# Optimization experiments

Measured on AMD Instinct MI355X. Metric: run time of the kernel, lower is better.

Reference implementation:

```python
import jax, jax.numpy as jnp
import numpy as np

EMBED = 1024
HEADS = 16
HEAD_DIM = EMBED // HEADS


def setup_inputs() -> dict:
    key = jax.random.key(0)
    ks = jax.random.split(key, 8)
    N, S = 4, 2048
    return {
        "keys": jax.random.normal(ks[0], (N, S, EMBED), dtype=jnp.float32),
        "query": jax.random.normal(ks[1], (N, S, EMBED), dtype=jnp.float32),
        "values": jax.random.normal(ks[2], (N, S, EMBED), dtype=jnp.float32),
        "Wk": jax.random.normal(ks[3], (HEAD_DIM, HEAD_DIM), dtype=jnp.float32) / np.sqrt(HEAD_DIM),
        "Wq": jax.random.normal(ks[4], (HEAD_DIM, HEAD_DIM), dtype=jnp.float32) / np.sqrt(HEAD_DIM),
        "Wv": jax.random.normal(ks[5], (HEAD_DIM, HEAD_DIM), dtype=jnp.float32) / np.sqrt(HEAD_DIM),
        "Wo": jax.random.normal(ks[6], (EMBED, EMBED), dtype=jnp.float32) / np.sqrt(EMBED),
        "bo": jax.random.normal(ks[7], (EMBED,), dtype=jnp.float32) * 0.01,
    }


def reference(keys, query, values, Wk, Wq, Wv, Wo, bo):
    N, Q, _ = query.shape
    K = keys.shape[1]
    # split heads: [n, s, h, d]
    k = keys.reshape(N, K, HEADS, HEAD_DIM) @ Wk.T
    q = query.reshape(N, Q, HEADS, HEAD_DIM) @ Wq.T
    v = values.reshape(N, K, HEADS, HEAD_DIM) @ Wv.T
    energy = jnp.einsum("nqhd,nkhd->nhqk", q, k)
    # NOTE: original torch code scales by embed_size**1 / 2 == embed_size/2 (quirk, kept faithful)
    attention = jax.nn.softmax(energy / (EMBED / 2), axis=3)
    out = jnp.einsum("nhqk,nkhd->nqhd", attention, v).reshape(N, Q, EMBED)
    return out @ Wo.T + bo
```

## Files before the change

### kernel.cpp

```cpp
#include <hip/hip_runtime.h>
#include <hip/hip_bf16.h>

#define HEADS 16
#define HDIM 64
#define EMB 1024
#define NBATCH 4
#define SEQ 2048
#define NT (SEQ/64)

typedef __bf16 bf16x8 __attribute__((ext_vector_type(8)));
typedef __bf16 bf16x4 __attribute__((ext_vector_type(4)));
typedef float f32x4 __attribute__((ext_vector_type(4)));
typedef float f32x16 __attribute__((ext_vector_type(16)));

#define Z16 {0.f,0.f,0.f,0.f,0.f,0.f,0.f,0.f,0.f,0.f,0.f,0.f,0.f,0.f,0.f,0.f}

static __device__ __forceinline__ bf16x8 load_cvt8(const float* __restrict__ p) {
    float4 a = *reinterpret_cast<const float4*>(p);
    float4 b = *reinterpret_cast<const float4*>(p + 4);
    bf16x8 r;
    r[0] = (__bf16)a.x; r[1] = (__bf16)a.y; r[2] = (__bf16)a.z; r[3] = (__bf16)a.w;
    r[4] = (__bf16)b.x; r[5] = (__bf16)b.y; r[6] = (__bf16)b.z; r[7] = (__bf16)b.w;
    return r;
}

static __device__ __forceinline__ unsigned cvt_pk_bf16(float a, float b) {
    unsigned d;
    asm("v_cvt_pk_bf16_f32 %0, %1, %2" : "=v"(d) : "v"(a), "v"(b));
    return d;
}

static __device__ __forceinline__ void pl_swap(unsigned &a, unsigned &b) {
#if __has_builtin(__builtin_amdgcn_permlane32_swap)
    auto r = __builtin_amdgcn_permlane32_swap((int)a, (int)b, false, false);
    a = (unsigned)r[0]; b = (unsigned)r[1];
#else
    asm("v_permlane32_swap_b32 %0, %1" : "+v"(a), "+v"(b));
#endif
}

__global__ __launch_bounds__(256) void proj_kernel(
    const float* __restrict__ keys, const float* __restrict__ query,
    const float* __restrict__ values,
    const float* __restrict__ Wk, const float* __restrict__ Wq,
    const float* __restrict__ Wv, const float* __restrict__ Wo,
    __bf16* __restrict__ qb, __bf16* __restrict__ kb, __bf16* __restrict__ vtb,
    __bf16* __restrict__ wob)
{
    int t = threadIdx.x;
    int which = blockIdx.z;

    if (which == 3) {
        int idx = blockIdx.y*gridDim.x + blockIdx.x;
        if (idx < EMB*EMB/4/256) {
            int i = idx*256 + t;
            float4 v = reinterpret_cast<const float4*>(Wo)[i];
            bf16x4 r;
            r[0] = (__bf16)v.x; r[1] = (__bf16)v.y; r[2] = (__bf16)v.z; r[3] = (__bf16)v.w;
            reinterpret_cast<bf16x4*>(wob)[i] = r;
        }
        return;
    }

    __shared__ __align__(16) __bf16 vlds[64][72];

    int wave = t >> 6, lane = t & 63;
    int l16 = lane & 15, g = lane >> 4;
    int sblk = blockIdx.x, nh = blockIdx.y;
    int n = nh >> 4, h = nh & 15;

    const float* X = (which == 0) ? query : (which == 1) ? keys : values;
    const float* W = (which == 0) ? Wq    : (which == 1) ? Wk   : Wv;
    const float wsc = (which == 0) ? (1.44269504088896f / 512.f) : 1.0f;

    {
        const float* wp = W + t*16;
        int row = t >> 2, c0 = (t & 3)*16;
#pragma unroll
        for (int q4 = 0; q4 < 4; ++q4) {
            float4 v = *reinterpret_cast<const float4*>(wp + q4*4);
            vlds[row][c0 + q4*4 + 0] = (__bf16)(v.x*wsc);
            vlds[row][c0 + q4*4 + 1] = (__bf16)(v.y*wsc);
            vlds[row][c0 + q4*4 + 2] = (__bf16)(v.z*wsc);
            vlds[row][c0 + q4*4 + 3] = (__bf16)(v.w*wsc);
        }
    }
    __syncthreads();

    bf16x8 wf[4][2];
#pragma unroll
    for (int j = 0; j < 4; ++j)
#pragma unroll
        for (int kc = 0; kc < 2; ++kc)
            wf[j][kc] = *reinterpret_cast<const bf16x8*>(&vlds[j*16 + l16][kc*32 + g*8]);

    int s0 = sblk*64 + wave*16;
    const float* xp = X + ((size_t)(n*SEQ + s0 + l16)*HEADS + h)*64;
    bf16x8 af0 = load_cvt8(xp + g*8);
    bf16x8 af1 = load_cvt8(xp + 32 + g*8);

    __syncthreads();

    f32x4 acc[4];
#pragma unroll
    for (int j = 0; j < 4; ++j) acc[j] = (f32x4){0.f, 0.f, 0.f, 0.f};
#pragma unroll
    for (int j = 0; j < 4; ++j) {
        acc[j] = __builtin_amdgcn_mfma_f32_16x16x32_bf16(af0, wf[j][0], acc[j], 0, 0, 0);
        acc[j] = __builtin_amdgcn_mfma_f32_16x16x32_bf16(af1, wf[j][1], acc[j], 0, 0, 0);
    }

#pragma unroll
    for (int j = 0; j < 4; ++j)
#pragma unroll
        for (int r = 0; r < 4; ++r)
            vlds[wave*16 + g*4 + r][j*16 + l16] = (__bf16)acc[j][r];
    __syncthreads();

    if (which < 2) {
        int row = t >> 2, seg = t & 3;
        __bf16* dst = (which == 0 ? qb : kb) + (size_t)nh*SEQ*64
                      + (size_t)(sblk*64 + row)*64 + seg*16;
        *reinterpret_cast<int4*>(dst)     = *reinterpret_cast<const int4*>(&vlds[row][seg*16]);
        *reinterpret_cast<int4*>(dst + 8) = *reinterpret_cast<const int4*>(&vlds[row][seg*16 + 8]);
    } else {
        int d = t & 63, sc4 = t >> 6;
        alignas(16) __bf16 tmp[16];
#pragma unroll
        for (int i = 0; i < 16; ++i) tmp[i] = vlds[sc4*16 + i][d];
        __bf16* dst = vtb + ((size_t)nh*64 + d)*SEQ + sblk*64 + sc4*16;
        *reinterpret_cast<int4*>(dst)     = *reinterpret_cast<const int4*>(tmp);
        *reinterpret_cast<int4*>(dst + 8) = *reinterpret_cast<const int4*>(tmp + 8);
    }
}

__global__ __launch_bounds__(256, 2) void attn_kernel(
    const __bf16* __restrict__ qb, const __bf16* __restrict__ kb,
    const __bf16* __restrict__ vtb, __bf16* __restrict__ ob)
{
    __shared__ __align__(16) char smem[49152];

    int t = threadIdx.x;
    int wave = t >> 6, lane = t & 63;
    int l31 = lane & 31, hi = lane >> 5;

    int id = blockIdx.x;
    int qblk = id >> 6;
    int nh = (id & 7)*8 + ((id >> 3) & 7);
    int n = nh >> 4, h = nh & 15;

    const __bf16* Qp = qb  + (size_t)nh*SEQ*64;
    const __bf16* Kp = kb  + (size_t)nh*SEQ*64;
    const __bf16* Vp = vtb + (size_t)nh*64*SEQ;

    int st_row[2], st_col[2];
#pragma unroll
    for (int i = 0; i < 2; ++i) {
        int o = wave*2048 + i*1024 + lane*16;
        st_row[i] = o >> 7;
        st_col[i] = (o & 127) ^ ((st_row[i] & 7) << 4);
    }

    int q0 = qblk*256 + wave*64;
    const __bf16* qp = Qp + (size_t)(q0 + l31)*64 + hi*8;
    bf16x8 qfA[4], qfB[4];
#pragma unroll
    for (int i = 0; i < 4; ++i) {
        qfA[i] = *reinterpret_cast<const bf16x8*>(qp + i*16);
        qfB[i] = *reinterpret_cast<const bf16x8*>(qp + 2048 + i*16);
    }

    f32x16 oaccA0 = Z16, oaccA1 = Z16, oaccB0 = Z16, oaccB1 = Z16;
    float lsA0 = 0.f, lsA1 = 0.f, lsA2 = 0.f, lsA3 = 0.f;
    float lsB0 = 0.f, lsB1 = 0.f, lsB2 = 0.f, lsB3 = 0.f;

#define STAGE_TILE(gbase, stride, ldsoff)                                          \
    {                                                                              \
        _Pragma("unroll")                                                          \
        for (int i_ = 0; i_ < 2; ++i_) {                                           \
            const char* g_ = (const char*)((gbase) + (size_t)st_row[i_]*(stride))  \
                             + st_col[i_];                                         \
            __builtin_amdgcn_global_load_lds(                                      \
                (const __attribute__((address_space(1))) void*)g_,                 \
                (__attribute__((address_space(3))) void*)(smem + (ldsoff)          \
                    + wave*2048 + i_*1024), 16, 0, 0);                             \
        }                                                                          \
    }

#define QKT(SB, EA, EB)                                                            \
    {                                                                              \
        bf16x8 kf0_ = *(const bf16x8*)(kb_ + ((SB)*32 + l31)*128 + ((0*32 + hi*16) ^ swz)); \
        bf16x8 kf1_ = *(const bf16x8*)(kb_ + ((SB)*32 + l31)*128 + ((1*32 + hi*16) ^ swz)); \
        bf16x8 kf2_ = *(const bf16x8*)(kb_ + ((SB)*32 + l31)*128 + ((2*32 + hi*16) ^ swz)); \
        bf16x8 kf3_ = *(const bf16x8*)(kb_ + ((SB)*32 + l31)*128 + ((3*32 + hi*16) ^ swz)); \
        __builtin_amdgcn_s_setprio(1);                                             \
        EA = __builtin_amdgcn_mfma_f32_32x32x16_bf16(kf0_, qfA[0], EA, 0, 0, 0);   \
        EB = __builtin_amdgcn_mfma_f32_32x32x16_bf16(kf0_, qfB[0], EB, 0, 0, 0);   \
        EA = __builtin_amdgcn_mfma_f32_32x32x16_bf16(kf1_, qfA[1], EA, 0, 0, 0);   \
        EB = __builtin_amdgcn_mfma_f32_32x32x16_bf16(kf1_, qfB[1], EB, 0, 0, 0);   \
        EA = __builtin_amdgcn_mfma_f32_32x32x16_bf16(kf2_, qfA[2], EA, 0, 0, 0);   \
        EB = __builtin_amdgcn_mfma_f32_32x32x16_bf16(kf2_, qfB[2], EB, 0, 0, 0);   \
        EA = __builtin_amdgcn_mfma_f32_32x32x16_bf16(kf3_, qfA[3], EA, 0, 0, 0);   \
        EB = __builtin_amdgcn_mfma_f32_32x32x16_bf16(kf3_, qfB[3], EB, 0, 0, 0);   \
        __builtin_amdgcn_s_setprio(0);                                             \
    }

#define MAKE_PU(E, LS0, LS1, LS2, LS3, PU0, PU1)                                   \
    {                                                                              \
        float p_[16];                                                              \
        _Pragma("unroll")                                                          \
        for (int i_ = 0; i_ < 16; ++i_)                                            \
            p_[i_] = __builtin_amdgcn_exp2f(E[i_]);                                \
        LS0 += p_[0] + p_[4];  LS1 += p_[1] + p_[5];                               \
        LS2 += p_[2] + p_[6];  LS3 += p_[3] + p_[7];                               \
        LS0 += p_[8] + p_[12]; LS1 += p_[9] + p_[13];                              \
        LS2 += p_[10] + p_[14]; LS3 += p_[11] + p_[15];                            \
        unsigned w00 = cvt_pk_bf16(p_[0],  p_[1]);                                 \
        unsigned w01 = cvt_pk_bf16(p_[2],  p_[3]);                                 \
        unsigned w10 = cvt_pk_bf16(p_[4],  p_[5]);                                 \
        unsigned w11 = cvt_pk_bf16(p_[6],  p_[7]);                                 \
        unsigned w20 = cvt_pk_bf16(p_[8],  p_[9]);                                 \
        unsigned w21 = cvt_pk_bf16(p_[10], p_[11]);                                \
        unsigned w30 = cvt_pk_bf16(p_[12], p_[13]);                                \
        unsigned w31 = cvt_pk_bf16(p_[14], p_[15]);                                \
        pl_swap(w00, w10); pl_swap(w01, w11);                                      \
        pl_swap(w20, w30); pl_swap(w21, w31);                                      \
        PU0.u[0] = w00; PU0.u[1] = w01; PU0.u[2] = w10; PU0.u[3] = w11;            \
        PU1.u[0] = w20; PU1.u[1] = w21; PU1.u[2] = w30; PU1.u[3] = w31;            \
    }

#define SMPV(SB, EA, EB)                                                           \
    {                                                                              \
        union { unsigned u[4]; bf16x8 v; } puA0, puA1, puB0, puB1;                 \
        MAKE_PU(EA, lsA0, lsA1, lsA2, lsA3, puA0, puA1)                            \
        MAKE_PU(EB, lsB0, lsB1, lsB2, lsB3, puB0, puB1)                            \
        bf16x8 v00 = *(const bf16x8*)(vb_ + (l31)*128      + (((SB)*64 +  0 + hi*16) ^ swz)); \
        bf16x8 v01 = *(const bf16x8*)(vb_ + (l31)*128      + (((SB)*64 + 32 + hi*16) ^ swz)); \
        bf16x8 v10 = *(const bf16x8*)(vb_ + (32 + l31)*128 + (((SB)*64 +  0 + hi*16) ^ swz)); \
        bf16x8 v11 = *(const bf16x8*)(vb_ + (32 + l31)*128 + (((SB)*64 + 32 + hi*16) ^ swz)); \
        __builtin_amdgcn_s_setprio(1);                                             \
        oaccA0 = __builtin_amdgcn_mfma_f32_32x32x16_bf16(v00, puA0.v, oaccA0, 0, 0, 0); \
        oaccA0 = __builtin_amdgcn_mfma_f32_32x32x16_bf16(v01, puA1.v, oaccA0, 0, 0, 0); \
        oaccA1 = __builtin_amdgcn_mfma_f32_32x32x16_bf16(v10, puA0.v, oaccA1, 0, 0, 0); \
        oaccA1 = __builtin_amdgcn_mfma_f32_32x32x16_bf16(v11, puA1.v, oaccA1, 0, 0, 0); \
        oaccB0 = __builtin_amdgcn_mfma_f32_32x32x16_bf16(v00, puB0.v, oaccB0, 0, 0, 0); \
        oaccB0 = __builtin_amdgcn_mfma_f32_32x32x16_bf16(v01, puB1.v, oaccB0, 0, 0, 0); \
        oaccB1 = __builtin_amdgcn_mfma_f32_32x32x16_bf16(v10, puB0.v, oaccB1, 0, 0, 0); \
        oaccB1 = __builtin_amdgcn_mfma_f32_32x32x16_bf16(v11, puB1.v, oaccB1, 0, 0, 0); \
        __builtin_amdgcn_s_setprio(0);                                             \
    }

    STAGE_TILE(Kp, 64, 0);
    STAGE_TILE(Vp, SEQ, 24576);
    STAGE_TILE(Kp + (size_t)64*64, 64, 8192);
    STAGE_TILE(Vp + 64, SEQ, 24576 + 8192);

    int cur = 0;
    for (int kt = 0; kt < NT; ++kt) {
        if (kt + 2 < NT) {
            int b2 = cur + 2; if (b2 >= 3) b2 -= 3;
            const __bf16* knext = Kp + (size_t)(kt + 2)*64*64;
            const __bf16* vnext = Vp + (size_t)(kt + 2)*64;
            STAGE_TILE(knext, 64, b2*8192);
            STAGE_TILE(vnext, SEQ, 24576 + b2*8192);
        }
        if (kt < NT - 2)       asm volatile("s_waitcnt vmcnt(8)" ::: "memory");
        else if (kt == NT - 2) asm volatile("s_waitcnt vmcnt(4)" ::: "memory");
        else                   asm volatile("s_waitcnt vmcnt(0)" ::: "memory");
        __builtin_amdgcn_s_barrier();
        __builtin_amdgcn_sched_barrier(0);

        const char* kb_ = smem + cur*8192;
        const char* vb_ = smem + 24576 + cur*8192;
        int swz = (l31 & 7) << 4;

        f32x16 eA0 = Z16, eB0 = Z16, eA1 = Z16, eB1 = Z16;
        QKT(0, eA0, eB0)
        QKT(1, eA1, eB1)
        __builtin_amdgcn_sched_barrier(0);
        SMPV(0, eA0, eB0)
        SMPV(1, eA1, eB1)

        __builtin_amdgcn_sched_barrier(0);
        asm volatile("" ::: "memory");
        __builtin_amdgcn_s_barrier();

        cur = (cur == 2) ? 0 : cur + 1;
    }

    float lA = (lsA0 + lsA1) + (lsA2 + lsA3);
    float totA = lA + __shfl_xor(lA, 32);
    float invA = 1.f / totA;
    float lB = (lsB0 + lsB1) + (lsB2 + lsB3);
    float totB = lB + __shfl_xor(lB, 32);
    float invB = 1.f / totB;

    __bf16* opA = ob + (size_t)(n*SEQ + q0 + l31)*EMB + h*64;
    __bf16* opB = opA + (size_t)32*EMB;
#pragma unroll
    for (int j = 0; j < 4; ++j)
#pragma unroll
        for (int c = 0; c < 4; ++c) {
            int d_ = c + 8*j + 4*hi;
            opA[d_]      = (__bf16)(oaccA0[4*j + c] * invA);
            opA[32 + d_] = (__bf16)(oaccA1[4*j + c] * invA);
            opB[d_]      = (__bf16)(oaccB0[4*j + c] * invB);
            opB[32 + d_] = (__bf16)(oaccB1[4*j + c] * invB);
        }
#undef STAGE_TILE
#undef QKT
#undef MAKE_PU
#undef SMPV
}

__global__ __launch_bounds__(256, 2) void out_gemm_kernel(
    const __bf16* __restrict__ ob, const __bf16* __restrict__ wob,
    const float* __restrict__ bo, float* __restrict__ out)
{
    __shared__ __align__(16) char smem[65536];

    int t = threadIdx.x;
    int wave = t >> 6, lane = t & 63;
    int l16 = lane & 15, g = lane >> 4;

    int bid = blockIdx.x;
    int swz = (bid & 7)*64 + (bid >> 3);
    int mb = (swz >> 3)*128;
    int nb = (swz & 7)*128;
    int wr = wave >> 1, wc = wave & 1;

    int st_row[4], st_col[4];
#pragma unroll
    for (int i = 0; i < 4; ++i) {
        int o = i*4096 + wave*1024 + lane*16;
        st_row[i] = o >> 7;
        st_col[i] = (o & 127) ^ ((st_row[i] & 7) << 4);
    }

#define G_STAGE(kt, buf)                                                            \
    {                                                                               \
        _Pragma("unroll")                                                           \
        for (int i_ = 0; i_ < 4; ++i_) {                                            \
            const char* ga_ = (const char*)(ob + (size_t)(mb + st_row[i_])*EMB      \
                                + (kt)*64) + st_col[i_];                            \
            __builtin_amdgcn_global_load_lds(                                       \
                (const __attribute__((address_space(1))) void*)ga_,                 \
                (__attribute__((address_space(3))) void*)(smem + (buf)*16384        \
                    + i_*4096 + wave*1024), 16, 0, 0);                              \
            const char* gb_ = (const char*)(wob + (size_t)(nb + st_row[i_])*EMB     \
                                + (kt)*64) + st_col[i_];                            \
            __builtin_amdgcn_global_load_lds(                                       \
                (const __attribute__((address_space(1))) void*)gb_,                 \
                (__attribute__((address_space(3))) void*)(smem + 32768 + (buf)*16384\
                    + i_*4096 + wave*1024), 16, 0, 0);                              \
        }                                                                           \
    }

    f32x4 acc[4][4];
#pragma unroll
    for (int m = 0; m < 4; ++m)
#pragma unroll
        for (int n = 0; n < 4; ++n) acc[m][n] = (f32x4){0.f, 0.f, 0.f, 0.f};

    G_STAGE(0, 0);
    __syncthreads();

    int cur = 0;
    for (int kt = 0; kt < EMB/64; ++kt) {
        if (kt + 1 < EMB/64) G_STAGE(kt + 1, cur ^ 1);

        const char* ab_ = smem + cur*16384;
        const char* bb_ = smem + 32768 + cur*16384;

        bf16x8 af[4][2], bf[4][2];
#pragma unroll
        for (int m = 0; m < 4; ++m) {
            int row = wr*64 + m*16 + l16, s = (row & 7) << 4;
            af[m][0] = *(const bf16x8*)(ab_ + row*128 + ((g*16) ^ s));
            af[m][1] = *(const bf16x8*)(ab_ + row*128 + ((64 + g*16) ^ s));
        }
#pragma unroll
        for (int n = 0; n < 4; ++n) {
            int row = wc*64 + n*16 + l16, s = (row & 7) << 4;
            bf[n][0] = *(const bf16x8*)(bb_ + row*128 + ((g*16) ^ s));
            bf[n][1] = *(const bf16x8*)(bb_ + row*128 + ((64 + g*16) ^ s));
        }

        __builtin_amdgcn_s_setprio(1);
#pragma unroll
        for (int m = 0; m < 4; ++m)
#pragma unroll
            for (int n = 0; n < 4; ++n) {
                acc[m][n] = __builtin_amdgcn_mfma_f32_16x16x32_bf16(af[m][0], bf[n][0], acc[m][n], 0, 0, 0);
                acc[m][n] = __builtin_amdgcn_mfma_f32_16x16x32_bf16(af[m][1], bf[n][1], acc[m][n], 0, 0, 0);
            }
        __builtin_amdgcn_s_setprio(0);

        __syncthreads();
        cur ^= 1;
    }

#pragma unroll
    for (int n = 0; n < 4; ++n) {
        int col = nb + wc*64 + n*16 + l16;
        float bias = bo[col];
#pragma unroll
        for (int m = 0; m < 4; ++m) {
            int rowb = mb + wr*64 + m*16 + g*4;
#pragma unroll
            for (int r = 0; r < 4; ++r)
                out[(size_t)(rowb + r)*EMB + col] = acc[m][n][r] + bias;
        }
    }
#undef G_STAGE
}

extern "C" void kernel_launch(void* const* d_in, const int* in_sizes, int n_in,
                              void* d_out, int out_size, void* d_ws, size_t ws_size,
                              hipStream_t stream) {
    const float* keys   = (const float*)d_in[0];
    const float* query  = (const float*)d_in[1];
    const float* values = (const float*)d_in[2];
    const float* Wk     = (const float*)d_in[3];
    const float* Wq     = (const float*)d_in[4];
    const float* Wv     = (const float*)d_in[5];
    const float* Wo     = (const float*)d_in[6];
    const float* bo     = (const float*)d_in[7];
    float* out = (float*)d_out;

    char* ws = (char*)d_ws;
    __bf16* qb  = (__bf16*)(ws);
    __bf16* kb  = (__bf16*)(ws + (size_t)16*1024*1024);
    __bf16* vtb = (__bf16*)(ws + (size_t)32*1024*1024);
    __bf16* ob  = (__bf16*)(ws + (size_t)48*1024*1024);
    __bf16* wob = (__bf16*)(ws + (size_t)64*1024*1024);

    hipLaunchKernelGGL(proj_kernel, dim3(SEQ/64, NBATCH*HEADS, 4), dim3(256), 0, stream,
                       keys, query, values, Wk, Wq, Wv, Wo, qb, kb, vtb, wob);
    hipLaunchKernelGGL(attn_kernel, dim3(512), dim3(256), 0, stream,
                       qb, kb, vtb, ob);
    hipLaunchKernelGGL(out_gemm_kernel, dim3(512), dim3(256), 0, stream,
                       ob, wob, bo, out);
}
```

Before: 126.7 us.

## Halve attention query tile per wave and double grid for higher occupancy

The attention kernel now gives each wave 32 query rows instead of 64. Each block therefore covers 128 queries, and the grid doubles to 1024 blocks. Launch bounds are raised to allow 3 blocks per CU, to cut register pressure and add latency hiding. In exchange, each staged K/V tile is reused by half as many queries, which doubles K/V load traffic. Each wave also has fewer independent MFMA chains, and 1024 blocks no longer divide evenly into the available CU slots, leaving a tail.

```diff
diff --git a/kernel.cpp b/kernel.cpp
--- a/kernel.cpp
+++ b/kernel.cpp
@@ -134,7 +134,7 @@
     }
 }
 
-__global__ __launch_bounds__(256, 2) void attn_kernel(
+__global__ __launch_bounds__(256, 3) void attn_kernel(
     const __bf16* __restrict__ qb, const __bf16* __restrict__ kb,
     const __bf16* __restrict__ vtb, __bf16* __restrict__ ob)
 {
@@ -161,18 +161,15 @@
         st_col[i] = (o & 127) ^ ((st_row[i] & 7) << 4);
     }
 
-    int q0 = qblk*256 + wave*64;
+    int q0 = qblk*128 + wave*32;
     const __bf16* qp = Qp + (size_t)(q0 + l31)*64 + hi*8;
-    bf16x8 qfA[4], qfB[4];
-#pragma unroll
-    for (int i = 0; i < 4; ++i) {
-        qfA[i] = *reinterpret_cast<const bf16x8*>(qp + i*16);
-        qfB[i] = *reinterpret_cast<const bf16x8*>(qp + 2048 + i*16);
-    }
-
-    f32x16 oaccA0 = Z16, oaccA1 = Z16, oaccB0 = Z16, oaccB1 = Z16;
-    float lsA0 = 0.f, lsA1 = 0.f, lsA2 = 0.f, lsA3 = 0.f;
-    float lsB0 = 0.f, lsB1 = 0.f, lsB2 = 0.f, lsB3 = 0.f;
+    bf16x8 qf[4];
+#pragma unroll
+    for (int i = 0; i < 4; ++i)
+        qf[i] = *reinterpret_cast<const bf16x8*>(qp + i*16);
+
+    f32x16 oacc0 = Z16, oacc1 = Z16;
+    float ls0 = 0.f, ls1 = 0.f, ls2 = 0.f, ls3 = 0.f;
 
 #define STAGE_TILE(gbase, stride, ldsoff)                                          \
     {                                                                              \
@@ -187,21 +184,17 @@
         }                                                                          \
     }
 
-#define QKT(SB, EA, EB)                                                            \
+#define QKT(SB, E)                                                                 \
     {                                                                              \
         bf16x8 kf0_ = *(const bf16x8*)(kb_ + ((SB)*32 + l31)*128 + ((0*32 + hi*16) ^ swz)); \
         bf16x8 kf1_ = *(const bf16x8*)(kb_ + ((SB)*32 + l31)*128 + ((1*32 + hi*16) ^ swz)); \
         bf16x8 kf2_ = *(const bf16x8*)(kb_ + ((SB)*32 + l31)*128 + ((2*32 + hi*16) ^ swz)); \
         bf16x8 kf3_ = *(const bf16x8*)(kb_ + ((SB)*32 + l31)*128 + ((3*32 + hi*16) ^ swz)); \
         __builtin_amdgcn_s_setprio(1);                                             \
-        EA = __builtin_amdgcn_mfma_f32_32x32x16_bf16(kf0_, qfA[0], EA, 0, 0, 0);   \
-        EB = __builtin_amdgcn_mfma_f32_32x32x16_bf16(kf0_, qfB[0], EB, 0, 0, 0);   \
-        EA = __builtin_amdgcn_mfma_f32_32x32x16_bf16(kf1_, qfA[1], EA, 0, 0, 0);   \
-        EB = __builtin_amdgcn_mfma_f32_32x32x16_bf16(kf1_, qfB[1], EB, 0, 0, 0);   \
-        EA = __builtin_amdgcn_mfma_f32_32x32x16_bf16(kf2_, qfA[2], EA, 0, 0, 0);   \
-        EB = __builtin_amdgcn_mfma_f32_32x32x16_bf16(kf2_, qfB[2], EB, 0, 0, 0);   \
-        EA = __builtin_amdgcn_mfma_f32_32x32x16_bf16(kf3_, qfA[3], EA, 0, 0, 0);   \
-        EB = __builtin_amdgcn_mfma_f32_32x32x16_bf16(kf3_, qfB[3], EB, 0, 0, 0);   \
+        E = __builtin_amdgcn_mfma_f32_32x32x16_bf16(kf0_, qf[0], E, 0, 0, 0);      \
+        E = __builtin_amdgcn_mfma_f32_32x32x16_bf16(kf1_, qf[1], E, 0, 0, 0);      \
+        E = __builtin_amdgcn_mfma_f32_32x32x16_bf16(kf2_, qf[2], E, 0, 0, 0);      \
+        E = __builtin_amdgcn_mfma_f32_32x32x16_bf16(kf3_, qf[3], E, 0, 0, 0);      \
         __builtin_amdgcn_s_setprio(0);                                             \
     }
 
@@ -229,24 +222,19 @@
         PU1.u[0] = w20; PU1.u[1] = w21; PU1.u[2] = w30; PU1.u[3] = w31;            \
     }
 
-#define SMPV(SB, EA, EB)                                                           \
+#define SMPV(SB, E)                                                                \
     {                                                                              \
-        union { unsigned u[4]; bf16x8 v; } puA0, puA1, puB0, puB1;                 \
-        MAKE_PU(EA, lsA0, lsA1, lsA2, lsA3, puA0, puA1)                            \
-        MAKE_PU(EB, lsB0, lsB1, lsB2, lsB3, puB0, puB1)                            \
+        union { unsigned u[4]; bf16x8 v; } pu0, pu1;                               \
+        MAKE_PU(E, ls0, ls1, ls2, ls3, pu0, pu1)                                   \
         bf16x8 v00 = *(const bf16x8*)(vb_ + (l31)*128      + (((SB)*64 +  0 + hi*16) ^ swz)); \
         bf16x8 v01 = *(const bf16x8*)(vb_ + (l31)*128      + (((SB)*64 + 32 + hi*16) ^ swz)); \
         bf16x8 v10 = *(const bf16x8*)(vb_ + (32 + l31)*128 + (((SB)*64 +  0 + hi*16) ^ swz)); \
         bf16x8 v11 = *(const bf16x8*)(vb_ + (32 + l31)*128 + (((SB)*64 + 32 + hi*16) ^ swz)); \
         __builtin_amdgcn_s_setprio(1);                                             \
-        oaccA0 = __builtin_amdgcn_mfma_f32_32x32x16_bf16(v00, puA0.v, oaccA0, 0, 0, 0); \
-        oaccA0 = __builtin_amdgcn_mfma_f32_32x32x16_bf16(v01, puA1.v, oaccA0, 0, 0, 0); \
-        oaccA1 = __builtin_amdgcn_mfma_f32_32x32x16_bf16(v10, puA0.v, oaccA1, 0, 0, 0); \
-        oaccA1 = __builtin_amdgcn_mfma_f32_32x32x16_bf16(v11, puA1.v, oaccA1, 0, 0, 0); \
-        oaccB0 = __builtin_amdgcn_mfma_f32_32x32x16_bf16(v00, puB0.v, oaccB0, 0, 0, 0); \
-        oaccB0 = __builtin_amdgcn_mfma_f32_32x32x16_bf16(v01, puB1.v, oaccB0, 0, 0, 0); \
-        oaccB1 = __builtin_amdgcn_mfma_f32_32x32x16_bf16(v10, puB0.v, oaccB1, 0, 0, 0); \
-        oaccB1 = __builtin_amdgcn_mfma_f32_32x32x16_bf16(v11, puB1.v, oaccB1, 0, 0, 0); \
+        oacc0 = __builtin_amdgcn_mfma_f32_32x32x16_bf16(v00, pu0.v, oacc0, 0, 0, 0); \
+        oacc0 = __builtin_amdgcn_mfma_f32_32x32x16_bf16(v01, pu1.v, oacc0, 0, 0, 0); \
+        oacc1 = __builtin_amdgcn_mfma_f32_32x32x16_bf16(v10, pu0.v, oacc1, 0, 0, 0); \
+        oacc1 = __builtin_amdgcn_mfma_f32_32x32x16_bf16(v11, pu1.v, oacc1, 0, 0, 0); \
         __builtin_amdgcn_s_setprio(0);                                             \
     }
 
@@ -274,12 +262,12 @@
         const char* vb_ = smem + 24576 + cur*8192;
         int swz = (l31 & 7) << 4;
 
-        f32x16 eA0 = Z16, eB0 = Z16, eA1 = Z16, eB1 = Z16;
-        QKT(0, eA0, eB0)
-        QKT(1, eA1, eB1)
+        f32x16 e0 = Z16, e1 = Z16;
+        QKT(0, e0)
+        QKT(1, e1)
         __builtin_amdgcn_sched_barrier(0);
-        SMPV(0, eA0, eB0)
-        SMPV(1, eA1, eB1)
+        SMPV(0, e0)
+        SMPV(1, e1)
 
         __builtin_amdgcn_sched_barrier(0);
         asm volatile("" ::: "memory");
@@ -288,24 +276,18 @@
         cur = (cur == 2) ? 0 : cur + 1;
     }
 
-    float lA = (lsA0 + lsA1) + (lsA2 + lsA3);
-    float totA = lA + __shfl_xor(lA, 32);
-    float invA = 1.f / totA;
-    float lB = (lsB0 + lsB1) + (lsB2 + lsB3);
-    float totB = lB + __shfl_xor(lB, 32);
-    float invB = 1.f / totB;
-
-    __bf16* opA = ob + (size_t)(n*SEQ + q0 + l31)*EMB + h*64;
-    __bf16* opB = opA + (size_t)32*EMB;
+    float l = (ls0 + ls1) + (ls2 + ls3);
+    float tot = l + __shfl_xor(l, 32);
+    float inv = 1.f / tot;
+
+    __bf16* op = ob + (size_t)(n*SEQ + q0 + l31)*EMB + h*64;
 #pragma unroll
     for (int j = 0; j < 4; ++j)
 #pragma unroll
         for (int c = 0; c < 4; ++c) {
             int d_ = c + 8*j + 4*hi;
-            opA[d_]      = (__bf16)(oaccA0[4*j + c] * invA);
-            opA[32 + d_] = (__bf16)(oaccA1[4*j + c] * invA);
-            opB[d_]      = (__bf16)(oaccB0[4*j + c] * invB);
-            opB[32 + d_] = (__bf16)(oaccB1[4*j + c] * invB);
+            op[d_]      = (__bf16)(oacc0[4*j + c] * inv);
+            op[32 + d_] = (__bf16)(oacc1[4*j + c] * inv);
         }
 #undef STAGE_TILE
 #undef QKT
@@ -437,7 +419,7 @@
 
     hipLaunchKernelGGL(proj_kernel, dim3(SEQ/64, NBATCH*HEADS, 4), dim3(256), 0, stream,
                        keys, query, values, Wk, Wq, Wv, Wo, qb, kb, vtb, wob);
-    hipLaunchKernelGGL(attn_kernel, dim3(512), dim3(256), 0, stream,
+    hipLaunchKernelGGL(attn_kernel, dim3(1024), dim3(256), 0, stream,
                        qb, kb, vtb, ob);
     hipLaunchKernelGGL(out_gemm_kernel, dim3(512), dim3(256), 0, stream,
                        ob, wob, bo, out);
```

Measured after the change: 132.2 us. 1.04x slower.

## Load K/V fragments directly from global into registers, drop LDS staging

Applied to the files above, without the earlier changes.

The attention kernel no longer stages K and V tiles through a triple-buffered LDS ring with global_load_lds and barriers. Each wave now loads its MFMA fragments straight from global memory into registers, prefetching the next tile's fragments after the current tile's MFMAs. This removes LDS traffic, barriers and waitcnt management, and frees shared memory. In exchange, the four waves of a block each fetch the same K/V data separately, which relies on L1/L2 caching. The V loads are strided by rows of SEQ, and latency hiding now depends on one-tile register prefetch, which also raises register pressure.

```diff
diff --git a/kernel.cpp b/kernel.cpp
--- a/kernel.cpp
+++ b/kernel.cpp
@@ -138,8 +138,6 @@
     const __bf16* __restrict__ qb, const __bf16* __restrict__ kb,
     const __bf16* __restrict__ vtb, __bf16* __restrict__ ob)
 {
-    __shared__ __align__(16) char smem[49152];
-
     int t = threadIdx.x;
     int wave = t >> 6, lane = t & 63;
     int l31 = lane & 31, hi = lane >> 5;
@@ -149,17 +147,9 @@
     int nh = (id & 7)*8 + ((id >> 3) & 7);
     int n = nh >> 4, h = nh & 15;
 
-    const __bf16* Qp = qb  + (size_t)nh*SEQ*64;
-    const __bf16* Kp = kb  + (size_t)nh*SEQ*64;
-    const __bf16* Vp = vtb + (size_t)nh*64*SEQ;
-
-    int st_row[2], st_col[2];
-#pragma unroll
-    for (int i = 0; i < 2; ++i) {
-        int o = wave*2048 + i*1024 + lane*16;
-        st_row[i] = o >> 7;
-        st_col[i] = (o & 127) ^ ((st_row[i] & 7) << 4);
-    }
+    const __bf16* Qp = qb + (size_t)nh*SEQ*64;
+    const char* Kp = (const char*)(kb  + (size_t)nh*SEQ*64);
+    const char* Vp = (const char*)(vtb + (size_t)nh*64*SEQ);
 
     int q0 = qblk*256 + wave*64;
     const __bf16* qp = Qp + (size_t)(q0 + l31)*64 + hi*8;
@@ -170,38 +160,40 @@
         qfB[i] = *reinterpret_cast<const bf16x8*>(qp + 2048 + i*16);
     }
 
-    f32x16 oaccA0 = Z16, oaccA1 = Z16, oaccB0 = Z16, oaccB1 = Z16;
-    float lsA0 = 0.f, lsA1 = 0.f, lsA2 = 0.f, lsA3 = 0.f;
-    float lsB0 = 0.f, lsB1 = 0.f, lsB2 = 0.f, lsB3 = 0.f;
-
-#define STAGE_TILE(gbase, stride, ldsoff)                                          \
+    const char* kBase = Kp + (size_t)l31*128 + hi*16;
+    const char* vBase = Vp + (size_t)l31*(SEQ*2) + hi*16;
+
+    bf16x8 kf0[4], kf1[4];
+    bf16x8 vf0[4], vf1[4];
+
+#define LOADK(kt, sb, dst)                                                         \
     {                                                                              \
-        _Pragma("unroll")                                                          \
-        for (int i_ = 0; i_ < 2; ++i_) {                                           \
-            const char* g_ = (const char*)((gbase) + (size_t)st_row[i_]*(stride))  \
-                             + st_col[i_];                                         \
-            __builtin_amdgcn_global_load_lds(                                      \
-                (const __attribute__((address_space(1))) void*)g_,                 \
-                (__attribute__((address_space(3))) void*)(smem + (ldsoff)          \
-                    + wave*2048 + i_*1024), 16, 0, 0);                             \
-        }                                                                          \
-    }
-
-#define QKT(SB, EA, EB)                                                            \
+        const char* p_ = kBase + ((size_t)(kt)*64 + (sb)*32)*128;                  \
+        dst[0] = *(const bf16x8*)(p_);                                             \
+        dst[1] = *(const bf16x8*)(p_ + 32);                                        \
+        dst[2] = *(const bf16x8*)(p_ + 64);                                        \
+        dst[3] = *(const bf16x8*)(p_ + 96);                                        \
+    }
+#define LOADV(kt, sb, dst)                                                         \
     {                                                                              \
-        bf16x8 kf0_ = *(const bf16x8*)(kb_ + ((SB)*32 + l31)*128 + ((0*32 + hi*16) ^ swz)); \
-        bf16x8 kf1_ = *(const bf16x8*)(kb_ + ((SB)*32 + l31)*128 + ((1*32 + hi*16) ^ swz)); \
-        bf16x8 kf2_ = *(const bf16x8*)(kb_ + ((SB)*32 + l31)*128 + ((2*32 + hi*16) ^ swz)); \
-        bf16x8 kf3_ = *(const bf16x8*)(kb_ + ((SB)*32 + l31)*128 + ((3*32 + hi*16) ^ swz)); \
+        const char* p_ = vBase + (size_t)(kt)*128 + (sb)*64;                       \
+        dst[0] = *(const bf16x8*)(p_);                                             \
+        dst[1] = *(const bf16x8*)(p_ + 32);                                        \
+        dst[2] = *(const bf16x8*)(p_ + (size_t)32*SEQ*2);                          \
+        dst[3] = *(const bf16x8*)(p_ + (size_t)32*SEQ*2 + 32);                     \
+    }
+
+#define QKT(KF, EA, EB)                                                            \
+    {                                                                              \
         __builtin_amdgcn_s_setprio(1);                                             \
-        EA = __builtin_amdgcn_mfma_f32_32x32x16_bf16(kf0_, qfA[0], EA, 0, 0, 0);   \
-        EB = __builtin_amdgcn_mfma_f32_32x32x16_bf16(kf0_, qfB[0], EB, 0, 0, 0);   \
-        EA = __builtin_amdgcn_mfma_f32_32x32x16_bf16(kf1_, qfA[1], EA, 0, 0, 0);   \
-        EB = __builtin_amdgcn_mfma_f32_32x32x16_bf16(kf1_, qfB[1], EB, 0, 0, 0);   \
-        EA = __builtin_amdgcn_mfma_f32_32x32x16_bf16(kf2_, qfA[2], EA, 0, 0, 0);   \
-        EB = __builtin_amdgcn_mfma_f32_32x32x16_bf16(kf2_, qfB[2], EB, 0, 0, 0);   \
-        EA = __builtin_amdgcn_mfma_f32_32x32x16_bf16(kf3_, qfA[3], EA, 0, 0, 0);   \
-        EB = __builtin_amdgcn_mfma_f32_32x32x16_bf16(kf3_, qfB[3], EB, 0, 0, 0);   \
+        EA = __builtin_amdgcn_mfma_f32_32x32x16_bf16(KF[0], qfA[0], EA, 0, 0, 0);  \
+        EB = __builtin_amdgcn_mfma_f32_32x32x16_bf16(KF[0], qfB[0], EB, 0, 0, 0);  \
+        EA = __builtin_amdgcn_mfma_f32_32x32x16_bf16(KF[1], qfA[1], EA, 0, 0, 0);  \
+        EB = __builtin_amdgcn_mfma_f32_32x32x16_bf16(KF[1], qfB[1], EB, 0, 0, 0);  \
+        EA = __builtin_amdgcn_mfma_f32_32x32x16_bf16(KF[2], qfA[2], EA, 0, 0, 0);  \
+        EB = __builtin_amdgcn_mfma_f32_32x32x16_bf16(KF[2], qfB[2], EB, 0, 0, 0);  \
+        EA = __builtin_amdgcn_mfma_f32_32x32x16_bf16(KF[3], qfA[3], EA, 0, 0, 0);  \
+        EB = __builtin_amdgcn_mfma_f32_32x32x16_bf16(KF[3], qfB[3], EB, 0, 0, 0);  \
         __builtin_amdgcn_s_setprio(0);                                             \
     }
 
@@ -229,63 +221,44 @@
         PU1.u[0] = w20; PU1.u[1] = w21; PU1.u[2] = w30; PU1.u[3] = w31;            \
     }
 
-#define SMPV(SB, EA, EB)                                                           \
+#define SMPV(VF, EA, EB)                                                           \
     {                                                                              \
         union { unsigned u[4]; bf16x8 v; } puA0, puA1, puB0, puB1;                 \
         MAKE_PU(EA, lsA0, lsA1, lsA2, lsA3, puA0, puA1)                            \
         MAKE_PU(EB, lsB0, lsB1, lsB2, lsB3, puB0, puB1)                            \
-        bf16x8 v00 = *(const bf16x8*)(vb_ + (l31)*128      + (((SB)*64 +  0 + hi*16) ^ swz)); \
-        bf16x8 v01 = *(const bf16x8*)(vb_ + (l31)*128      + (((SB)*64 + 32 + hi*16) ^ swz)); \
-        bf16x8 v10 = *(const bf16x8*)(vb_ + (32 + l31)*128 + (((SB)*64 +  0 + hi*16) ^ swz)); \
-        bf16x8 v11 = *(const bf16x8*)(vb_ + (32 + l31)*128 + (((SB)*64 + 32 + hi*16) ^ swz)); \
         __builtin_amdgcn_s_setprio(1);                                             \
-        oaccA0 = __builtin_amdgcn_mfma_f32_32x32x16_bf16(v00, puA0.v, oaccA0, 0, 0, 0); \
-        oaccA0 = __builtin_amdgcn_mfma_f32_32x32x16_bf16(v01, puA1.v, oaccA0, 0, 0, 0); \
-        oaccA1 = __builtin_amdgcn_mfma_f32_32x32x16_bf16(v10, puA0.v, oaccA1, 0, 0, 0); \
-        oaccA1 = __builtin_amdgcn_mfma_f32_32x32x16_bf16(v11, puA1.v, oaccA1, 0, 0, 0); \
-        oaccB0 = __builtin_amdgcn_mfma_f32_32x32x16_bf16(v00, puB0.v, oaccB0, 0, 0, 0); \
-        oaccB0 = __builtin_amdgcn_mfma_f32_32x32x16_bf16(v01, puB1.v, oaccB0, 0, 0, 0); \
-        oaccB1 = __builtin_amdgcn_mfma_f32_32x32x16_bf16(v10, puB0.v, oaccB1, 0, 0, 0); \
-        oaccB1 = __builtin_amdgcn_mfma_f32_32x32x16_bf16(v11, puB1.v, oaccB1, 0, 0, 0); \
+        oaccA0 = __builtin_amdgcn_mfma_f32_32x32x16_bf16(VF[0], puA0.v, oaccA0, 0, 0, 0); \
+        oaccA0 = __builtin_amdgcn_mfma_f32_32x32x16_bf16(VF[1], puA1.v, oaccA0, 0, 0, 0); \
+        oaccA1 = __builtin_amdgcn_mfma_f32_32x32x16_bf16(VF[2], puA0.v, oaccA1, 0, 0, 0); \
+        oaccA1 = __builtin_amdgcn_mfma_f32_32x32x16_bf16(VF[3], puA1.v, oaccA1, 0, 0, 0); \
+        oaccB0 = __builtin_amdgcn_mfma_f32_32x32x16_bf16(VF[0], puB0.v, oaccB0, 0, 0, 0); \
+        oaccB0 = __builtin_amdgcn_mfma_f32_32x32x16_bf16(VF[1], puB1.v, oaccB0, 0, 0, 0); \
+        oaccB1 = __builtin_amdgcn_mfma_f32_32x32x16_bf16(VF[2], puB0.v, oaccB1, 0, 0, 0); \
+        oaccB1 = __builtin_amdgcn_mfma_f32_32x32x16_bf16(VF[3], puB1.v, oaccB1, 0, 0, 0); \
         __builtin_amdgcn_s_setprio(0);                                             \
     }
 
-    STAGE_TILE(Kp, 64, 0);
-    STAGE_TILE(Vp, SEQ, 24576);
-    STAGE_TILE(Kp + (size_t)64*64, 64, 8192);
-    STAGE_TILE(Vp + 64, SEQ, 24576 + 8192);
-
-    int cur = 0;
+    f32x16 oaccA0 = Z16, oaccA1 = Z16, oaccB0 = Z16, oaccB1 = Z16;
+    float lsA0 = 0.f, lsA1 = 0.f, lsA2 = 0.f, lsA3 = 0.f;
+    float lsB0 = 0.f, lsB1 = 0.f, lsB2 = 0.f, lsB3 = 0.f;
+
+    LOADK(0, 0, kf0); LOADK(0, 1, kf1);
+    LOADV(0, 0, vf0); LOADV(0, 1, vf1);
+
     for (int kt = 0; kt < NT; ++kt) {
-        if (kt + 2 < NT) {
-            int b2 = cur + 2; if (b2 >= 3) b2 -= 3;
-            const __bf16* knext = Kp + (size_t)(kt + 2)*64*64;
-            const __bf16* vnext = Vp + (size_t)(kt + 2)*64;
-            STAGE_TILE(knext, 64, b2*8192);
-            STAGE_TILE(vnext, SEQ, 24576 + b2*8192);
-        }
-        if (kt < NT - 2)       asm volatile("s_waitcnt vmcnt(8)" ::: "memory");
-        else if (kt == NT - 2) asm volatile("s_waitcnt vmcnt(4)" ::: "memory");
-        else                   asm volatile("s_waitcnt vmcnt(0)" ::: "memory");
-        __builtin_amdgcn_s_barrier();
-        __builtin_amdgcn_sched_barrier(0);
-
-        const char* kb_ = smem + cur*8192;
-        const char* vb_ = smem + 24576 + cur*8192;
-        int swz = (l31 & 7) << 4;
+        int nx = (kt + 1 < NT) ? kt + 1 : kt;
 
         f32x16 eA0 = Z16, eB0 = Z16, eA1 = Z16, eB1 = Z16;
-        QKT(0, eA0, eB0)
-        QKT(1, eA1, eB1)
-        __builtin_amdgcn_sched_barrier(0);
-        SMPV(0, eA0, eB0)
-        SMPV(1, eA1, eB1)
-
-        __builtin_amdgcn_sched_barrier(0);
-        asm volatile("" ::: "memory");
-        __builtin_amdgcn_s_barrier();
-
-        cur = (cur == 2) ? 0 : cur + 1;
+
+        QKT(kf0, eA0, eB0)
+        LOADK(nx, 0, kf0)
+        QKT(kf1, eA1, eB1)
+        LOADK(nx, 1, kf1)
+
+        SMPV(vf0, eA0, eB0)
+        LOADV(nx, 0, vf0)
+        SMPV(vf1, eA1, eB1)
+        LOADV(nx, 1, vf1)
     }
 
     float lA = (lsA0 + lsA1) + (lsA2 + lsA3);
@@ -307,7 +280,8 @@
             opB[d_]      = (__bf16)(oaccB0[4*j + c] * invB);
             opB[32 + d_] = (__bf16)(oaccB1[4*j + c] * invB);
         }
-#undef STAGE_TILE
+#undef LOADK
+#undef LOADV
 #undef QKT
 #undef MAKE_PU
 #undef SMPV
```

Result: slower. 202.5 us (+59.9%).

## Use four-slot LDS ring to drop trailing barrier and interleave MFMA chains

Applied to the files above, without the earlier changes.

Changes the K/V LDS staging ring from three to four slots (LDS grows to 64KB) so the end-of-iteration barrier can be removed. The prefetch two tiles ahead can no longer overwrite a slot that slower waves are still reading. It also merges the two QK^T blocks so four independent accumulator chains interleave, reorders the PV MFMAs so consecutive ones do not depend on each other, and moves the row-sum accumulation after the MFMAs. The extra LDS may limit occupancy at 2 blocks per CU, and the longer live ranges of the probability arrays add register pressure.

```diff
diff --git a/kernel.cpp b/kernel.cpp
--- a/kernel.cpp
+++ b/kernel.cpp
@@ -138,7 +138,7 @@
     const __bf16* __restrict__ qb, const __bf16* __restrict__ kb,
     const __bf16* __restrict__ vtb, __bf16* __restrict__ ob)
 {
-    __shared__ __align__(16) char smem[49152];
+    __shared__ __align__(16) char smem[65536];
 
     int t = threadIdx.x;
     int wave = t >> 6, lane = t & 63;
@@ -187,82 +187,99 @@
         }                                                                          \
     }
 
-#define QKT(SB, EA, EB)                                                            \
+#define QKT2()                                                                     \
     {                                                                              \
-        bf16x8 kf0_ = *(const bf16x8*)(kb_ + ((SB)*32 + l31)*128 + ((0*32 + hi*16) ^ swz)); \
-        bf16x8 kf1_ = *(const bf16x8*)(kb_ + ((SB)*32 + l31)*128 + ((1*32 + hi*16) ^ swz)); \
-        bf16x8 kf2_ = *(const bf16x8*)(kb_ + ((SB)*32 + l31)*128 + ((2*32 + hi*16) ^ swz)); \
-        bf16x8 kf3_ = *(const bf16x8*)(kb_ + ((SB)*32 + l31)*128 + ((3*32 + hi*16) ^ swz)); \
+        bf16x8 k00_ = *(const bf16x8*)(kb_ + (l31)*128      + ((0*32 + hi*16) ^ swz)); \
+        bf16x8 k01_ = *(const bf16x8*)(kb_ + (l31)*128      + ((1*32 + hi*16) ^ swz)); \
+        bf16x8 k02_ = *(const bf16x8*)(kb_ + (l31)*128      + ((2*32 + hi*16) ^ swz)); \
+        bf16x8 k03_ = *(const bf16x8*)(kb_ + (l31)*128      + ((3*32 + hi*16) ^ swz)); \
+        bf16x8 k10_ = *(const bf16x8*)(kb_ + (32 + l31)*128 + ((0*32 + hi*16) ^ swz)); \
+        bf16x8 k11_ = *(const bf16x8*)(kb_ + (32 + l31)*128 + ((1*32 + hi*16) ^ swz)); \
+        bf16x8 k12_ = *(const bf16x8*)(kb_ + (32 + l31)*128 + ((2*32 + hi*16) ^ swz)); \
+        bf16x8 k13_ = *(const bf16x8*)(kb_ + (32 + l31)*128 + ((3*32 + hi*16) ^ swz)); \
         __builtin_amdgcn_s_setprio(1);                                             \
-        EA = __builtin_amdgcn_mfma_f32_32x32x16_bf16(kf0_, qfA[0], EA, 0, 0, 0);   \
-        EB = __builtin_amdgcn_mfma_f32_32x32x16_bf16(kf0_, qfB[0], EB, 0, 0, 0);   \
-        EA = __builtin_amdgcn_mfma_f32_32x32x16_bf16(kf1_, qfA[1], EA, 0, 0, 0);   \
-        EB = __builtin_amdgcn_mfma_f32_32x32x16_bf16(kf1_, qfB[1], EB, 0, 0, 0);   \
-        EA = __builtin_amdgcn_mfma_f32_32x32x16_bf16(kf2_, qfA[2], EA, 0, 0, 0);   \
-        EB = __builtin_amdgcn_mfma_f32_32x32x16_bf16(kf2_, qfB[2], EB, 0, 0, 0);   \
-        EA = __builtin_amdgcn_mfma_f32_32x32x16_bf16(kf3_, qfA[3], EA, 0, 0, 0);   \
-        EB = __builtin_amdgcn_mfma_f32_32x32x16_bf16(kf3_, qfB[3], EB, 0, 0, 0);   \
+        eA0 = __builtin_amdgcn_mfma_f32_32x32x16_bf16(k00_, qfA[0], eA0, 0, 0, 0); \
+        eB0 = __builtin_amdgcn_mfma_f32_32x32x16_bf16(k00_, qfB[0], eB0, 0, 0, 0); \
+        eA1 = __builtin_amdgcn_mfma_f32_32x32x16_bf16(k10_, qfA[0], eA1, 0, 0, 0); \
+        eB1 = __builtin_amdgcn_mfma_f32_32x32x16_bf16(k10_, qfB[0], eB1, 0, 0, 0); \
+        eA0 = __builtin_amdgcn_mfma_f32_32x32x16_bf16(k01_, qfA[1], eA0, 0, 0, 0); \
+        eB0 = __builtin_amdgcn_mfma_f32_32x32x16_bf16(k01_, qfB[1], eB0, 0, 0, 0); \
+        eA1 = __builtin_amdgcn_mfma_f32_32x32x16_bf16(k11_, qfA[1], eA1, 0, 0, 0); \
+        eB1 = __builtin_amdgcn_mfma_f32_32x32x16_bf16(k11_, qfB[1], eB1, 0, 0, 0); \
+        eA0 = __builtin_amdgcn_mfma_f32_32x32x16_bf16(k02_, qfA[2], eA0, 0, 0, 0); \
+        eB0 = __builtin_amdgcn_mfma_f32_32x32x16_bf16(k02_, qfB[2], eB0, 0, 0, 0); \
+        eA1 = __builtin_amdgcn_mfma_f32_32x32x16_bf16(k12_, qfA[2], eA1, 0, 0, 0); \
+        eB1 = __builtin_amdgcn_mfma_f32_32x32x16_bf16(k12_, qfB[2], eB1, 0, 0, 0); \
+        eA0 = __builtin_amdgcn_mfma_f32_32x32x16_bf16(k03_, qfA[3], eA0, 0, 0, 0); \
+        eB0 = __builtin_amdgcn_mfma_f32_32x32x16_bf16(k03_, qfB[3], eB0, 0, 0, 0); \
+        eA1 = __builtin_amdgcn_mfma_f32_32x32x16_bf16(k13_, qfA[3], eA1, 0, 0, 0); \
+        eB1 = __builtin_amdgcn_mfma_f32_32x32x16_bf16(k13_, qfB[3], eB1, 0, 0, 0); \
         __builtin_amdgcn_s_setprio(0);                                             \
     }
 
-#define MAKE_PU(E, LS0, LS1, LS2, LS3, PU0, PU1)                                   \
+#define MAKE_PU_FAST(E, P, PU0, PU1)                                               \
     {                                                                              \
-        float p_[16];                                                              \
         _Pragma("unroll")                                                          \
         for (int i_ = 0; i_ < 16; ++i_)                                            \
-            p_[i_] = __builtin_amdgcn_exp2f(E[i_]);                                \
-        LS0 += p_[0] + p_[4];  LS1 += p_[1] + p_[5];                               \
-        LS2 += p_[2] + p_[6];  LS3 += p_[3] + p_[7];                               \
-        LS0 += p_[8] + p_[12]; LS1 += p_[9] + p_[13];                              \
-        LS2 += p_[10] + p_[14]; LS3 += p_[11] + p_[15];                            \
-        unsigned w00 = cvt_pk_bf16(p_[0],  p_[1]);                                 \
-        unsigned w01 = cvt_pk_bf16(p_[2],  p_[3]);                                 \
-        unsigned w10 = cvt_pk_bf16(p_[4],  p_[5]);                                 \
-        unsigned w11 = cvt_pk_bf16(p_[6],  p_[7]);                                 \
-        unsigned w20 = cvt_pk_bf16(p_[8],  p_[9]);                                 \
-        unsigned w21 = cvt_pk_bf16(p_[10], p_[11]);                                \
-        unsigned w30 = cvt_pk_bf16(p_[12], p_[13]);                                \
-        unsigned w31 = cvt_pk_bf16(p_[14], p_[15]);                                \
+            P[i_] = __builtin_amdgcn_exp2f(E[i_]);                                 \
+        unsigned w00 = cvt_pk_bf16(P[0],  P[1]);                                   \
+        unsigned w01 = cvt_pk_bf16(P[2],  P[3]);                                   \
+        unsigned w10 = cvt_pk_bf16(P[4],  P[5]);                                   \
+        unsigned w11 = cvt_pk_bf16(P[6],  P[7]);                                   \
+        unsigned w20 = cvt_pk_bf16(P[8],  P[9]);                                   \
+        unsigned w21 = cvt_pk_bf16(P[10], P[11]);                                  \
+        unsigned w30 = cvt_pk_bf16(P[12], P[13]);                                  \
+        unsigned w31 = cvt_pk_bf16(P[14], P[15]);                                  \
         pl_swap(w00, w10); pl_swap(w01, w11);                                      \
         pl_swap(w20, w30); pl_swap(w21, w31);                                      \
         PU0.u[0] = w00; PU0.u[1] = w01; PU0.u[2] = w10; PU0.u[3] = w11;            \
         PU1.u[0] = w20; PU1.u[1] = w21; PU1.u[2] = w30; PU1.u[3] = w31;            \
     }
 
+#define LS_ACC(P, LS0, LS1, LS2, LS3)                                              \
+    {                                                                              \
+        LS0 += P[0] + P[4];  LS1 += P[1] + P[5];                                   \
+        LS2 += P[2] + P[6];  LS3 += P[3] + P[7];                                   \
+        LS0 += P[8] + P[12]; LS1 += P[9] + P[13];                                  \
+        LS2 += P[10] + P[14]; LS3 += P[11] + P[15];                                \
+    }
+
 #define SMPV(SB, EA, EB)                                                           \
     {                                                                              \
         union { unsigned u[4]; bf16x8 v; } puA0, puA1, puB0, puB1;                 \
-        MAKE_PU(EA, lsA0, lsA1, lsA2, lsA3, puA0, puA1)                            \
-        MAKE_PU(EB, lsB0, lsB1, lsB2, lsB3, puB0, puB1)                            \
+        float pA_[16], pB_[16];                                                    \
+        MAKE_PU_FAST(EA, pA_, puA0, puA1)                                          \
+        MAKE_PU_FAST(EB, pB_, puB0, puB1)                                          \
         bf16x8 v00 = *(const bf16x8*)(vb_ + (l31)*128      + (((SB)*64 +  0 + hi*16) ^ swz)); \
         bf16x8 v01 = *(const bf16x8*)(vb_ + (l31)*128      + (((SB)*64 + 32 + hi*16) ^ swz)); \
         bf16x8 v10 = *(const bf16x8*)(vb_ + (32 + l31)*128 + (((SB)*64 +  0 + hi*16) ^ swz)); \
         bf16x8 v11 = *(const bf16x8*)(vb_ + (32 + l31)*128 + (((SB)*64 + 32 + hi*16) ^ swz)); \
         __builtin_amdgcn_s_setprio(1);                                             \
         oaccA0 = __builtin_amdgcn_mfma_f32_32x32x16_bf16(v00, puA0.v, oaccA0, 0, 0, 0); \
+        oaccA1 = __builtin_amdgcn_mfma_f32_32x32x16_bf16(v10, puA0.v, oaccA1, 0, 0, 0); \
+        oaccB0 = __builtin_amdgcn_mfma_f32_32x32x16_bf16(v00, puB0.v, oaccB0, 0, 0, 0); \
+        oaccB1 = __builtin_amdgcn_mfma_f32_32x32x16_bf16(v10, puB0.v, oaccB1, 0, 0, 0); \
         oaccA0 = __builtin_amdgcn_mfma_f32_32x32x16_bf16(v01, puA1.v, oaccA0, 0, 0, 0); \
-        oaccA1 = __builtin_amdgcn_mfma_f32_32x32x16_bf16(v10, puA0.v, oaccA1, 0, 0, 0); \
         oaccA1 = __builtin_amdgcn_mfma_f32_32x32x16_bf16(v11, puA1.v, oaccA1, 0, 0, 0); \
-        oaccB0 = __builtin_amdgcn_mfma_f32_32x32x16_bf16(v00, puB0.v, oaccB0, 0, 0, 0); \
         oaccB0 = __builtin_amdgcn_mfma_f32_32x32x16_bf16(v01, puB1.v, oaccB0, 0, 0, 0); \
-        oaccB1 = __builtin_amdgcn_mfma_f32_32x32x16_bf16(v10, puB0.v, oaccB1, 0, 0, 0); \
         oaccB1 = __builtin_amdgcn_mfma_f32_32x32x16_bf16(v11, puB1.v, oaccB1, 0, 0, 0); \
         __builtin_amdgcn_s_setprio(0);                                             \
+        LS_ACC(pA_, lsA0, lsA1, lsA2, lsA3)                                        \
+        LS_ACC(pB_, lsB0, lsB1, lsB2, lsB3)                                        \
     }
 
     STAGE_TILE(Kp, 64, 0);
-    STAGE_TILE(Vp, SEQ, 24576);
+    STAGE_TILE(Vp, SEQ, 32768);
     STAGE_TILE(Kp + (size_t)64*64, 64, 8192);
-    STAGE_TILE(Vp + 64, SEQ, 24576 + 8192);
-
-    int cur = 0;
+    STAGE_TILE(Vp + 64, SEQ, 32768 + 8192);
+
     for (int kt = 0; kt < NT; ++kt) {
         if (kt + 2 < NT) {
-            int b2 = cur + 2; if (b2 >= 3) b2 -= 3;
+            int b2 = (kt + 2) & 3;
             const __bf16* knext = Kp + (size_t)(kt + 2)*64*64;
             const __bf16* vnext = Vp + (size_t)(kt + 2)*64;
             STAGE_TILE(knext, 64, b2*8192);
-            STAGE_TILE(vnext, SEQ, 24576 + b2*8192);
+            STAGE_TILE(vnext, SEQ, 32768 + b2*8192);
         }
         if (kt < NT - 2)       asm volatile("s_waitcnt vmcnt(8)" ::: "memory");
         else if (kt == NT - 2) asm volatile("s_waitcnt vmcnt(4)" ::: "memory");
@@ -270,22 +287,16 @@
         __builtin_amdgcn_s_barrier();
         __builtin_amdgcn_sched_barrier(0);
 
-        const char* kb_ = smem + cur*8192;
-        const char* vb_ = smem + 24576 + cur*8192;
+        const char* kb_ = smem + (kt & 3)*8192;
+        const char* vb_ = smem + 32768 + (kt & 3)*8192;
         int swz = (l31 & 7) << 4;
 
         f32x16 eA0 = Z16, eB0 = Z16, eA1 = Z16, eB1 = Z16;
-        QKT(0, eA0, eB0)
-        QKT(1, eA1, eB1)
+        QKT2()
         __builtin_amdgcn_sched_barrier(0);
         SMPV(0, eA0, eB0)
         SMPV(1, eA1, eB1)
-
         __builtin_amdgcn_sched_barrier(0);
-        asm volatile("" ::: "memory");
-        __builtin_amdgcn_s_barrier();
-
-        cur = (cur == 2) ? 0 : cur + 1;
     }
 
     float lA = (lsA0 + lsA1) + (lsA2 + lsA3);
@@ -308,8 +319,9 @@
             opB[32 + d_] = (__bf16)(oaccB1[4*j + c] * invB);
         }
 #undef STAGE_TILE
-#undef QKT
-#undef MAKE_PU
+#undef QKT2
+#undef MAKE_PU_FAST
+#undef LS_ACC
 #undef SMPV
 }
 
```

Result: slower. 129.3 us (+2.1%).
